# Kernel optimization log

Hardware: AMD Instinct MI355X
Metric: run time of the kernel (lower is better)

The kernel has to match this reference:

```python
import jax, jax.numpy as jnp
import numpy as np
from jax import lax

N, H, W, T = 8, 100, 152, 256
STRIDE = 8
ANCHOR_SIZE = 64.0
PRE_NMS_THRESH = 0.05
PRE_NMS_TOP_N = 1000
NMS_THRESH = 0.6
POST_TOP_N = 100
IMG_H, IMG_W = 800, 1216
BW = (10.0, 10.0, 5.0, 5.0)          # BoxCoder weights (wx, wy, ww, wh)
DWH_CLIP = float(np.log(1000.0 / 16.0))
TO_REMOVE = 1.0


def setup_inputs() -> dict:
    key = jax.random.key(0)
    k1, k2, k3 = jax.random.split(key, 3)
    box_regression = jax.random.normal(k1, (N, 4, H, W), dtype=jnp.float32)
    centerness = jax.random.normal(k2, (N, 1, H, W), dtype=jnp.float32)
    dot_product_logits = jax.random.normal(k3, (N, H * W, T), dtype=jnp.float32)
    # anchor grid matching permute_and_flatten's (H, W, A) row-major ordering
    ys, xs = jnp.meshgrid(jnp.arange(H, dtype=jnp.float32),
                          jnp.arange(W, dtype=jnp.float32), indexing="ij")
    cx = xs.reshape(-1) * STRIDE + STRIDE / 2.0
    cy = ys.reshape(-1) * STRIDE + STRIDE / 2.0
    half = ANCHOR_SIZE / 2.0
    anc = jnp.stack([cx - half, cy - half, cx + half, cy + half], axis=-1)  # [H*W, 4]
    anchors = jnp.broadcast_to(anc, (N, H * W, 4)).astype(jnp.float32)
    return {"box_regression": box_regression, "centerness": centerness,
            "anchors": anchors, "dot_product_logits": dot_product_logits}


def _decode(rel, anc):
    w = anc[..., 2] - anc[..., 0] + TO_REMOVE
    h = anc[..., 3] - anc[..., 1] + TO_REMOVE
    cx = anc[..., 0] + 0.5 * w
    cy = anc[..., 1] + 0.5 * h
    dx = rel[..., 0] / BW[0]
    dy = rel[..., 1] / BW[1]
    dw = jnp.minimum(rel[..., 2] / BW[2], DWH_CLIP)
    dh = jnp.minimum(rel[..., 3] / BW[3], DWH_CLIP)
    pcx = dx * w + cx
    pcy = dy * h + cy
    pw = jnp.exp(dw) * w
    ph = jnp.exp(dh) * h
    return jnp.stack([pcx - 0.5 * pw, pcy - 0.5 * ph,
                      pcx + 0.5 * pw - 1.0, pcy + 0.5 * ph - 1.0], axis=-1)


def _iou_one_vs_all(box, boxes):
    area1 = (box[2] - box[0] + TO_REMOVE) * (box[3] - box[1] + TO_REMOVE)
    area2 = (boxes[:, 2] - boxes[:, 0] + TO_REMOVE) * (boxes[:, 3] - boxes[:, 1] + TO_REMOVE)
    lt = jnp.maximum(box[:2], boxes[:, :2])
    rb = jnp.minimum(box[2:], boxes[:, 2:])
    wh = jnp.maximum(rb - lt + TO_REMOVE, 0.0)
    inter = wh[:, 0] * wh[:, 1]
    return inter / (area1 + area2 - inter)


def _nms_single(boxes, scores):
    # greedy NMS, fixed POST_TOP_N iterations (fpn_post_nms_top_n)
    def step(s, _):
        j = jnp.argmax(s)
        sj = s[j]
        bj = boxes[j]
        flag = (sj > 0).astype(boxes.dtype)
        ious = _iou_one_vs_all(bj, boxes)
        s = jnp.where(ious > NMS_THRESH, 0.0, s).at[j].set(0.0)
        return s, (bj * flag, sj * flag)
    _, (kb, ks) = lax.scan(step, scores, None, length=POST_TOP_N)
    return kb, ks


def reference(box_regression, centerness, anchors, dot_product_logits):
    n, _, h, w = box_regression.shape
    # sigmoid + MEAN token aggregation  -> [N, HWA]
    scores = jax.nn.sigmoid(dot_product_logits).mean(-1)
    # permute_and_flatten: [N,4A,H,W] -> [N, HWA, 4]
    box_reg = box_regression.reshape(n, 1, 4, h, w).transpose(0, 3, 4, 1, 2).reshape(n, -1, 4)
    ctr = jax.nn.sigmoid(centerness.reshape(n, 1, 1, h, w).transpose(0, 3, 4, 1, 2).reshape(n, -1))
    cand = scores > PRE_NMS_THRESH          # threshold on raw aggregated scores
    cls = scores * ctr                      # centerness-weighted score
    masked = jnp.where(cand, cls, 0.0)
    vals, idx = lax.top_k(masked, PRE_NMS_TOP_N)          # per-image top-k candidates
    valid = jnp.take_along_axis(cand, idx, axis=1)        # [N, PRE_NMS_TOP_N]
    sel_reg = jnp.take_along_axis(box_reg, idx[..., None], axis=1)
    sel_anc = jnp.take_along_axis(anchors, idx[..., None], axis=1)
    boxes = _decode(sel_reg, sel_anc)
    # clip_to_image
    boxes = jnp.stack([
        jnp.clip(boxes[..., 0], 0.0, IMG_W - 1.0),
        jnp.clip(boxes[..., 1], 0.0, IMG_H - 1.0),
        jnp.clip(boxes[..., 2], 0.0, IMG_W - 1.0),
        jnp.clip(boxes[..., 3], 0.0, IMG_H - 1.0)], axis=-1)
    vf = valid.astype(boxes.dtype)
    det_scores = jnp.sqrt(jnp.where(valid, vals, 1.0)) * vf   # sqrt of cls*ctr, safe grad
    keep_boxes, keep_scores = jax.vmap(_nms_single)(boxes, det_scores)
    return keep_boxes, keep_scores
```

## Files before the change

kernel.cpp:

```cpp
#include <hip/hip_runtime.h>
#include <math.h>

#define NN 8
#define HH 100
#define WW 152
#define HW (HH*WW)
#define TT 256
#define TOPN 1000
#define POSTN 100
#define NMS_T 0.6f
#define IMGW 1216
#define IMGH 800
#define DWH_CLIP 4.135166556742356f

typedef unsigned long long u64;
typedef unsigned int u32;

__global__ __launch_bounds__(256) void score_kernel(
    const float* __restrict__ logits,
    const float* __restrict__ centerness,
    float* __restrict__ masked)
{
    int wid  = blockIdx.x * 4 + (threadIdx.x >> 6);
    int lane = threadIdx.x & 63;
    const float4 v = *(reinterpret_cast<const float4*>(logits + (size_t)wid * TT) + lane);
    float s = 0.f;
    s += __fdividef(1.f, 1.f + expf(-v.x));
    s += __fdividef(1.f, 1.f + expf(-v.y));
    s += __fdividef(1.f, 1.f + expf(-v.z));
    s += __fdividef(1.f, 1.f + expf(-v.w));
    #pragma unroll
    for (int off = 32; off; off >>= 1) s += __shfl_xor(s, off, 64);
    if (lane == 0) {
        float score = s * (1.0f / 256.0f);
        float c = centerness[wid];
        float ctr = 1.f / (1.f + expf(-c));
        masked[wid] = (score > 0.05f) ? score * ctr : 0.f;
    }
}

__global__ __launch_bounds__(256) void select_nms_kernel(
    const float* __restrict__ masked,
    const float* __restrict__ box_reg,
    float* __restrict__ out)
{
    const int n   = blockIdx.x;
    const int tid = threadIdx.x;
    const int wv  = tid >> 6;
    const int PER = (HW + 255) / 256;

    u32 bits[PER];
    const float* mb = masked + (size_t)n * HW;
    #pragma unroll
    for (int j = 0; j < PER; j++) {
        int e = tid + j * 256;
        bits[j] = (e < HW) ? __float_as_uint(mb[e]) : 0u;
    }

    __shared__ int   parts[2][4];
    __shared__ u64   keys[256];
    __shared__ float4 sbox[256];
    __shared__ float  sscr[256];
    __shared__ int   s_cnt1, s_cnt2;
    __shared__ int   s_state;

    float* outb = out + (size_t)n * POSTN * 4;
    float* outs = out + (size_t)NN * POSTN * 4 + (size_t)n * POSTN;

    float ax1 = 0.f, ay1 = 0.f, ax2 = 0.f, ay2 = 0.f;
    float bx1 = 0.f, by1 = 0.f, bx2 = 0.f, by2 = 0.f;
    int   kept = 0;
    bool  done = false;

    u32 thrPrev = 0xFFFFFFFFu;
    int  p = 0;

    for (int b = 0; b < 4 && !done; ++b) {
        const int target = 256 * (b + 1) - 1;
        u32 lo = 0u;
        u32 hi = (thrPrev < 0x3F800000u) ? thrPrev : 0x3F800000u;
        while (lo < hi) {
            u32 mid = lo + ((hi - lo) >> 1);
            int c = 0;
            #pragma unroll
            for (int j = 0; j < PER; j++) c += (bits[j] > mid) ? 1 : 0;
            #pragma unroll
            for (int off = 32; off; off >>= 1) c += __shfl_xor(c, off, 64);
            if ((tid & 63) == 0) parts[p][wv] = c;
            __syncthreads();
            int tot = parts[p][0] + parts[p][1] + parts[p][2] + parts[p][3];
            p ^= 1;
            if (tot <= target) hi = mid; else lo = mid + 1;
        }
        const u32 thr = lo;

        if (tid == 0) { s_cnt1 = 0; s_cnt2 = 0; }
        keys[tid] = 0ull;
        __syncthreads();
        #pragma unroll
        for (int j = 0; j < PER; j++) {
            int e = tid + j * 256;
            u32 v = bits[j];
            if (e < HW && v > thr && v < thrPrev) {
                int pos = atomicAdd(&s_cnt1, 1);
                if (pos < 256) keys[pos] = (((u64)v) << 32) | (u32)(~e);
            }
        }
        __syncthreads();
        const int c1 = min(s_cnt1, 256);
        #pragma unroll
        for (int j = 0; j < PER; j++) {
            int e = tid + j * 256;
            if (e < HW && bits[j] == thr) {
                int q = atomicAdd(&s_cnt2, 1);
                if (c1 + q < 256) keys[c1 + q] = (((u64)thr) << 32) | (u32)(~e);
            }
        }
        __syncthreads();

        for (int k = 2; k <= 256; k <<= 1) {
            for (int j2 = k >> 1; j2 > 0; j2 >>= 1) {
                int ixj = tid ^ j2;
                if (ixj > tid) {
                    u64 a = keys[tid], bb = keys[ixj];
                    bool sw = ((tid & k) == 0) ? (a < bb) : (a > bb);
                    if (sw) { keys[tid] = bb; keys[ixj] = a; }
                }
                __syncthreads();
            }
        }

        {
            u64 kk = keys[tid];
            float s = __uint_as_float((u32)(kk >> 32));
            float4 box = make_float4(0.f, 0.f, 0.f, 0.f);
            float scr = 0.f;
            if (s > 0.f) {
                int loc = (int)(~(u32)kk);
                float acx = (float)(loc % WW) * 8.f + 4.f;
                float acy = (float)(loc / WW) * 8.f + 4.f;
                float a0 = acx - 32.f, a1 = acy - 32.f, a2 = acx + 32.f, a3 = acy + 32.f;
                float r0 = box_reg[((size_t)n * 4 + 0) * HW + loc];
                float r1 = box_reg[((size_t)n * 4 + 1) * HW + loc];
                float r2 = box_reg[((size_t)n * 4 + 2) * HW + loc];
                float r3 = box_reg[((size_t)n * 4 + 3) * HW + loc];
                float w  = a2 - a0 + 1.0f;
                float h  = a3 - a1 + 1.0f;
                float cx = a0 + 0.5f * w;
                float cy = a1 + 0.5f * h;
                float dx = r0 / 10.0f;
                float dy = r1 / 10.0f;
                float dw = fminf(r2 / 5.0f, DWH_CLIP);
                float dh = fminf(r3 / 5.0f, DWH_CLIP);
                float pcx = dx * w + cx;
                float pcy = dy * h + cy;
                float pw  = expf(dw) * w;
                float ph  = expf(dh) * h;
                float x1 = pcx - 0.5f * pw;
                float y1 = pcy - 0.5f * ph;
                float x2 = pcx + 0.5f * pw - 1.0f;
                float y2 = pcy + 0.5f * ph - 1.0f;
                box.x = fminf(fmaxf(x1, 0.f), (float)(IMGW - 1));
                box.y = fminf(fmaxf(y1, 0.f), (float)(IMGH - 1));
                box.z = fminf(fmaxf(x2, 0.f), (float)(IMGW - 1));
                box.w = fminf(fmaxf(y2, 0.f), (float)(IMGH - 1));
                scr = sqrtf(s);
            }
            sbox[tid] = box;
            sscr[tid] = scr;
        }
        __syncthreads();

        if (tid < 64) {
            const int limit = (b == 3) ? (TOPN - 3 * 256) : 256;
            for (int i = 0; i < limit; ++i) {
                float s = sscr[i];
                if (s <= 0.f) { done = true; break; }
                float4 cb = sbox[i];
                float carea = (cb.z - cb.x + 1.f) * (cb.w - cb.y + 1.f);

                float ix1 = fmaxf(cb.x, ax1), iy1 = fmaxf(cb.y, ay1);
                float ix2 = fminf(cb.z, ax2), iy2 = fminf(cb.w, ay2);
                float iw = fmaxf(ix2 - ix1 + 1.f, 0.f), ih = fmaxf(iy2 - iy1 + 1.f, 0.f);
                float interA = iw * ih;
                float areaA = (ax2 - ax1 + 1.f) * (ay2 - ay1 + 1.f);
                float iouA = interA / (carea + areaA - interA);

                ix1 = fmaxf(cb.x, bx1); iy1 = fmaxf(cb.y, by1);
                ix2 = fminf(cb.z, bx2); iy2 = fminf(cb.w, by2);
                iw = fmaxf(ix2 - ix1 + 1.f, 0.f); ih = fmaxf(iy2 - iy1 + 1.f, 0.f);
                float interB = iw * ih;
                float areaB = (bx2 - bx1 + 1.f) * (by2 - by1 + 1.f);
                float iouB = interB / (carea + areaB - interB);

                bool supA = (tid < kept)      && (iouA > NMS_T);
                bool supB = (tid < kept - 64) && (iouB > NMS_T);
                u64 sup = __ballot(supA) | __ballot(supB);
                if (sup == 0ull) {
                    if (kept < 64) {
                        if (tid == kept)      { ax1 = cb.x; ay1 = cb.y; ax2 = cb.z; ay2 = cb.w; }
                    } else {
                        if (tid == kept - 64) { bx1 = cb.x; by1 = cb.y; bx2 = cb.z; by2 = cb.w; }
                    }
                    if (tid == 0) {
                        outb[kept * 4 + 0] = cb.x; outb[kept * 4 + 1] = cb.y;
                        outb[kept * 4 + 2] = cb.z; outb[kept * 4 + 3] = cb.w;
                        outs[kept] = s;
                    }
                    ++kept;
                    if (kept == POSTN) { done = true; break; }
                }
            }
            if (tid == 0) s_state = kept | (done ? 0x10000 : 0);
        }
        __syncthreads();
        done = (s_state >> 16) != 0;
        thrPrev = thr;
    }

    const int cnt = s_state & 0xFFFF;
    for (int i = cnt + tid; i < POSTN; i += 256) {
        outb[i * 4 + 0] = 0.f; outb[i * 4 + 1] = 0.f;
        outb[i * 4 + 2] = 0.f; outb[i * 4 + 3] = 0.f;
        outs[i] = 0.f;
    }
}

extern "C" void kernel_launch(void* const* d_in, const int* in_sizes, int n_in,
                              void* d_out, int out_size, void* d_ws, size_t ws_size,
                              hipStream_t stream) {
    const float* box_reg = (const float*)d_in[0];
    const float* center  = (const float*)d_in[1];
    const float* logits  = (const float*)d_in[3];
    float* out = (float*)d_out;

    float* masked = (float*)d_ws;

    score_kernel<<<(NN * HW) / 4, 256, 0, stream>>>(logits, center, masked);
    select_nms_kernel<<<NN, 256, 0, stream>>>(masked, box_reg, out);
}
```

Before: 260.3 us.

## Replace batched bitonic-sort NMS with single-pass argmax-driven greedy NMS

Drops the four rounds of radix-threshold search, bitonic sort and sequential NMS over 256-candidate batches. It now does one threshold search for the top 1000, decodes every candidate once into shared memory, and runs greedy NMS in one wavefront. Each step takes a wave-wide argmax over packed score/index keys held in registers and then suppresses the remaining candidates with a division-free IoU test. This removes the sort barriers and the per-candidate serial loop; the cost is about 100 iterations of 16-candidate IoU per lane plus a shuffle reduction, and the double-precision comparison may be slow.

```diff
diff --git a/kernel.cpp b/kernel.cpp
--- a/kernel.cpp
+++ b/kernel.cpp
@@ -7,8 +7,8 @@
 #define HW (HH*WW)
 #define TT 256
 #define TOPN 1000
+#define CAP 1024
 #define POSTN 100
-#define NMS_T 0.6f
 #define IMGW 1216
 #define IMGH 800
 #define DWH_CLIP 4.135166556742356f
@@ -44,12 +44,13 @@
     const float* __restrict__ box_reg,
     float* __restrict__ out)
 {
-    const int n   = blockIdx.x;
-    const int tid = threadIdx.x;
-    const int wv  = tid >> 6;
-    const int PER = (HW + 255) / 256;
-
-    u32 bits[PER];
+    const int n    = blockIdx.x;
+    const int tid  = threadIdx.x;
+    const int wv   = tid >> 6;
+    const int lane = tid & 63;
+    const int PER  = (HW + 255) / 256;
+
+    u32 bits[(HW + 255) / 256];
     const float* mb = masked + (size_t)n * HW;
     #pragma unroll
     for (int j = 0; j < PER; j++) {
@@ -57,168 +58,169 @@
         bits[j] = (e < HW) ? __float_as_uint(mb[e]) : 0u;
     }
 
-    __shared__ int   parts[2][4];
-    __shared__ u64   keys[256];
-    __shared__ float4 sbox[256];
-    __shared__ float  sscr[256];
-    __shared__ int   s_cnt1, s_cnt2;
-    __shared__ int   s_state;
+    __shared__ int    parts[2][4];
+    __shared__ int    s_cnt1, s_cnt2, s_kept;
+    __shared__ float4 sbox[CAP];
+    __shared__ float  s_scr[CAP];
+    __shared__ float  s_area[CAP];
+    __shared__ u32    s_loc[CAP];
 
     float* outb = out + (size_t)n * POSTN * 4;
     float* outs = out + (size_t)NN * POSTN * 4 + (size_t)n * POSTN;
 
-    float ax1 = 0.f, ay1 = 0.f, ax2 = 0.f, ay2 = 0.f;
-    float bx1 = 0.f, by1 = 0.f, bx2 = 0.f, by2 = 0.f;
-    int   kept = 0;
-    bool  done = false;
-
-    u32 thrPrev = 0xFFFFFFFFu;
-    int  p = 0;
-
-    for (int b = 0; b < 4 && !done; ++b) {
-        const int target = 256 * (b + 1) - 1;
-        u32 lo = 0u;
-        u32 hi = (thrPrev < 0x3F800000u) ? thrPrev : 0x3F800000u;
-        while (lo < hi) {
-            u32 mid = lo + ((hi - lo) >> 1);
-            int c = 0;
-            #pragma unroll
-            for (int j = 0; j < PER; j++) c += (bits[j] > mid) ? 1 : 0;
-            #pragma unroll
-            for (int off = 32; off; off >>= 1) c += __shfl_xor(c, off, 64);
-            if ((tid & 63) == 0) parts[p][wv] = c;
-            __syncthreads();
-            int tot = parts[p][0] + parts[p][1] + parts[p][2] + parts[p][3];
-            p ^= 1;
-            if (tot <= target) hi = mid; else lo = mid + 1;
-        }
-        const u32 thr = lo;
-
-        if (tid == 0) { s_cnt1 = 0; s_cnt2 = 0; }
-        keys[tid] = 0ull;
+    int p = 0;
+    u32 lo = 0u, hi = 0x3F800000u;
+    while (lo < hi) {
+        u32 mid = lo + ((hi - lo) >> 1);
+        int c = 0;
+        #pragma unroll
+        for (int j = 0; j < PER; j++) c += (bits[j] > mid) ? 1 : 0;
+        #pragma unroll
+        for (int off = 32; off; off >>= 1) c += __shfl_xor(c, off, 64);
+        if (lane == 0) parts[p][wv] = c;
         __syncthreads();
-        #pragma unroll
-        for (int j = 0; j < PER; j++) {
-            int e = tid + j * 256;
-            u32 v = bits[j];
-            if (e < HW && v > thr && v < thrPrev) {
-                int pos = atomicAdd(&s_cnt1, 1);
-                if (pos < 256) keys[pos] = (((u64)v) << 32) | (u32)(~e);
-            }
-        }
-        __syncthreads();
-        const int c1 = min(s_cnt1, 256);
+        int tot = parts[p][0] + parts[p][1] + parts[p][2] + parts[p][3];
+        p ^= 1;
+        if (tot <= TOPN - 1) hi = mid; else lo = mid + 1;
+    }
+    const u32 thr = lo;
+
+    #pragma unroll
+    for (int j = 0; j < CAP / 256; j++) s_scr[tid + j * 256] = 0.f;
+    if (tid == 0) { s_cnt1 = 0; s_cnt2 = 0; }
+    __syncthreads();
+    #pragma unroll
+    for (int j = 0; j < PER; j++) {
+        int e = tid + j * 256;
+        u32 v = bits[j];
+        if (e < HW && v > thr) {
+            int pos = atomicAdd(&s_cnt1, 1);
+            if (pos < TOPN) { s_scr[pos] = __uint_as_float(v); s_loc[pos] = (u32)e; }
+        }
+    }
+    __syncthreads();
+    const int c1 = min(s_cnt1, TOPN);
+    if (thr > 0u) {
         #pragma unroll
         for (int j = 0; j < PER; j++) {
             int e = tid + j * 256;
             if (e < HW && bits[j] == thr) {
                 int q = atomicAdd(&s_cnt2, 1);
-                if (c1 + q < 256) keys[c1 + q] = (((u64)thr) << 32) | (u32)(~e);
-            }
-        }
-        __syncthreads();
-
-        for (int k = 2; k <= 256; k <<= 1) {
-            for (int j2 = k >> 1; j2 > 0; j2 >>= 1) {
-                int ixj = tid ^ j2;
-                if (ixj > tid) {
-                    u64 a = keys[tid], bb = keys[ixj];
-                    bool sw = ((tid & k) == 0) ? (a < bb) : (a > bb);
-                    if (sw) { keys[tid] = bb; keys[ixj] = a; }
-                }
-                __syncthreads();
-            }
-        }
-
-        {
-            u64 kk = keys[tid];
-            float s = __uint_as_float((u32)(kk >> 32));
-            float4 box = make_float4(0.f, 0.f, 0.f, 0.f);
-            float scr = 0.f;
-            if (s > 0.f) {
-                int loc = (int)(~(u32)kk);
-                float acx = (float)(loc % WW) * 8.f + 4.f;
-                float acy = (float)(loc / WW) * 8.f + 4.f;
-                float a0 = acx - 32.f, a1 = acy - 32.f, a2 = acx + 32.f, a3 = acy + 32.f;
-                float r0 = box_reg[((size_t)n * 4 + 0) * HW + loc];
-                float r1 = box_reg[((size_t)n * 4 + 1) * HW + loc];
-                float r2 = box_reg[((size_t)n * 4 + 2) * HW + loc];
-                float r3 = box_reg[((size_t)n * 4 + 3) * HW + loc];
-                float w  = a2 - a0 + 1.0f;
-                float h  = a3 - a1 + 1.0f;
-                float cx = a0 + 0.5f * w;
-                float cy = a1 + 0.5f * h;
-                float dx = r0 / 10.0f;
-                float dy = r1 / 10.0f;
-                float dw = fminf(r2 / 5.0f, DWH_CLIP);
-                float dh = fminf(r3 / 5.0f, DWH_CLIP);
-                float pcx = dx * w + cx;
-                float pcy = dy * h + cy;
-                float pw  = expf(dw) * w;
-                float ph  = expf(dh) * h;
-                float x1 = pcx - 0.5f * pw;
-                float y1 = pcy - 0.5f * ph;
-                float x2 = pcx + 0.5f * pw - 1.0f;
-                float y2 = pcy + 0.5f * ph - 1.0f;
-                box.x = fminf(fmaxf(x1, 0.f), (float)(IMGW - 1));
-                box.y = fminf(fmaxf(y1, 0.f), (float)(IMGH - 1));
-                box.z = fminf(fmaxf(x2, 0.f), (float)(IMGW - 1));
-                box.w = fminf(fmaxf(y2, 0.f), (float)(IMGH - 1));
-                scr = sqrtf(s);
-            }
-            sbox[tid] = box;
-            sscr[tid] = scr;
-        }
-        __syncthreads();
-
-        if (tid < 64) {
-            const int limit = (b == 3) ? (TOPN - 3 * 256) : 256;
-            for (int i = 0; i < limit; ++i) {
-                float s = sscr[i];
-                if (s <= 0.f) { done = true; break; }
-                float4 cb = sbox[i];
-                float carea = (cb.z - cb.x + 1.f) * (cb.w - cb.y + 1.f);
-
-                float ix1 = fmaxf(cb.x, ax1), iy1 = fmaxf(cb.y, ay1);
-                float ix2 = fminf(cb.z, ax2), iy2 = fminf(cb.w, ay2);
-                float iw = fmaxf(ix2 - ix1 + 1.f, 0.f), ih = fmaxf(iy2 - iy1 + 1.f, 0.f);
-                float interA = iw * ih;
-                float areaA = (ax2 - ax1 + 1.f) * (ay2 - ay1 + 1.f);
-                float iouA = interA / (carea + areaA - interA);
-
-                ix1 = fmaxf(cb.x, bx1); iy1 = fmaxf(cb.y, by1);
-                ix2 = fminf(cb.z, bx2); iy2 = fminf(cb.w, by2);
-                iw = fmaxf(ix2 - ix1 + 1.f, 0.f); ih = fmaxf(iy2 - iy1 + 1.f, 0.f);
-                float interB = iw * ih;
-                float areaB = (bx2 - bx1 + 1.f) * (by2 - by1 + 1.f);
-                float iouB = interB / (carea + areaB - interB);
-
-                bool supA = (tid < kept)      && (iouA > NMS_T);
-                bool supB = (tid < kept - 64) && (iouB > NMS_T);
-                u64 sup = __ballot(supA) | __ballot(supB);
-                if (sup == 0ull) {
-                    if (kept < 64) {
-                        if (tid == kept)      { ax1 = cb.x; ay1 = cb.y; ax2 = cb.z; ay2 = cb.w; }
-                    } else {
-                        if (tid == kept - 64) { bx1 = cb.x; by1 = cb.y; bx2 = cb.z; by2 = cb.w; }
-                    }
-                    if (tid == 0) {
-                        outb[kept * 4 + 0] = cb.x; outb[kept * 4 + 1] = cb.y;
-                        outb[kept * 4 + 2] = cb.z; outb[kept * 4 + 3] = cb.w;
-                        outs[kept] = s;
-                    }
-                    ++kept;
-                    if (kept == POSTN) { done = true; break; }
-                }
-            }
-            if (tid == 0) s_state = kept | (done ? 0x10000 : 0);
-        }
-        __syncthreads();
-        done = (s_state >> 16) != 0;
-        thrPrev = thr;
-    }
-
-    const int cnt = s_state & 0xFFFF;
+                int pos = c1 + q;
+                if (pos < TOPN) { s_scr[pos] = __uint_as_float(thr); s_loc[pos] = (u32)e; }
+            }
+        }
+    }
+    __syncthreads();
+
+    #pragma unroll
+    for (int j = 0; j < CAP / 256; j++) {
+        int slot = tid + j * 256;
+        float s = s_scr[slot];
+        float4 box = make_float4(0.f, 0.f, 0.f, 0.f);
+        float area = 0.f;
+        if (s > 0.f) {
+            int loc = (int)s_loc[slot];
+            float acx = (float)(loc % WW) * 8.f + 4.f;
+            float acy = (float)(loc / WW) * 8.f + 4.f;
+            float a0 = acx - 32.f, a1 = acy - 32.f, a2 = acx + 32.f, a3 = acy + 32.f;
+            float r0 = box_reg[((size_t)n * 4 + 0) * HW + loc];
+            float r1 = box_reg[((size_t)n * 4 + 1) * HW + loc];
+            float r2 = box_reg[((size_t)n * 4 + 2) * HW + loc];
+            float r3 = box_reg[((size_t)n * 4 + 3) * HW + loc];
+            float w  = a2 - a0 + 1.0f;
+            float h  = a3 - a1 + 1.0f;
+            float cx = a0 + 0.5f * w;
+            float cy = a1 + 0.5f * h;
+            float dx = r0 / 10.0f;
+            float dy = r1 / 10.0f;
+            float dw = fminf(r2 / 5.0f, DWH_CLIP);
+            float dh = fminf(r3 / 5.0f, DWH_CLIP);
+            float pcx = dx * w + cx;
+            float pcy = dy * h + cy;
+            float pw  = expf(dw) * w;
+            float ph  = expf(dh) * h;
+            float x1 = pcx - 0.5f * pw;
+            float y1 = pcy - 0.5f * ph;
+            float x2 = pcx + 0.5f * pw - 1.0f;
+            float y2 = pcy + 0.5f * ph - 1.0f;
+            box.x = fminf(fmaxf(x1, 0.f), (float)(IMGW - 1));
+            box.y = fminf(fmaxf(y1, 0.f), (float)(IMGH - 1));
+            box.z = fminf(fmaxf(x2, 0.f), (float)(IMGW - 1));
+            box.w = fminf(fmaxf(y2, 0.f), (float)(IMGH - 1));
+            area = (box.z - box.x + 1.0f) * (box.w - box.y + 1.0f);
+        }
+        sbox[slot]   = box;
+        s_area[slot] = area;
+    }
+    __syncthreads();
+
+    if (tid < 64) {
+        u64   key[16];
+        float cx1[16], cy1[16], cx2[16], cy2[16], car[16];
+        #pragma unroll
+        for (int r = 0; r < 16; r++) {
+            int slot = r * 64 + lane;
+            float s  = s_scr[slot];
+            float4 b = sbox[slot];
+            cx1[r] = b.x; cy1[r] = b.y; cx2[r] = b.z; cy2[r] = b.w;
+            car[r] = s_area[slot];
+            u32 loc = s_loc[slot];
+            key[r] = (s > 0.f)
+                ? ((((u64)__float_as_uint(s)) << 32)
+                   | ((u64)((16383u - loc) & 0x3FFFu) << 10)
+                   | (u64)slot)
+                : 0ull;
+        }
+
+        const double MD = (double)0.6f + 0x1p-25;
+        int kept = 0;
+        while (kept < POSTN) {
+            u64 t[8];
+            #pragma unroll
+            for (int r = 0; r < 8; r++) t[r] = (key[2*r] > key[2*r+1]) ? key[2*r] : key[2*r+1];
+            #pragma unroll
+            for (int r = 0; r < 4; r++) t[r] = (t[r] > t[r+4]) ? t[r] : t[r+4];
+            t[0] = (t[0] > t[2]) ? t[0] : t[2];
+            t[1] = (t[1] > t[3]) ? t[1] : t[3];
+            u64 m = (t[0] > t[1]) ? t[0] : t[1];
+            #pragma unroll
+            for (int off = 32; off; off >>= 1) {
+                u64 o = __shfl_xor(m, off, 64);
+                if (o > m) m = o;
+            }
+            if (m == 0ull) break;
+
+            const int   slot  = (int)(m & 1023u);
+            const float ws    = __uint_as_float((u32)(m >> 32));
+            const float4 wb   = sbox[slot];
+            const float warea = s_area[slot];
+            if (lane == 0) {
+                outb[kept * 4 + 0] = wb.x; outb[kept * 4 + 1] = wb.y;
+                outb[kept * 4 + 2] = wb.z; outb[kept * 4 + 3] = wb.w;
+                outs[kept] = sqrtf(ws);
+            }
+            if ((slot & 63) == lane) key[slot >> 6] = 0ull;
+            #pragma unroll
+            for (int r = 0; r < 16; r++) {
+                float ix1 = fmaxf(wb.x, cx1[r]);
+                float iy1 = fmaxf(wb.y, cy1[r]);
+                float ix2 = fminf(wb.z, cx2[r]);
+                float iy2 = fminf(wb.w, cy2[r]);
+                float iw = fmaxf(ix2 - ix1 + 1.0f, 0.0f);
+                float ih = fmaxf(iy2 - iy1 + 1.0f, 0.0f);
+                float inter = iw * ih;
+                float denom = (warea + car[r]) - inter;
+                bool sup = ((double)inter > MD * (double)denom);
+                key[r] = sup ? 0ull : key[r];
+            }
+            ++kept;
+        }
+        if (lane == 0) s_kept = kept;
+    }
+    __syncthreads();
+
+    const int cnt = s_kept;
     for (int i = cnt + tid; i < POSTN; i += 256) {
         outb[i * 4 + 0] = 0.f; outb[i * 4 + 1] = 0.f;
         outb[i * 4 + 2] = 0.f; outb[i * 4 + 3] = 0.f;
```

Result: slower. 336.5 us (+29.3%).

## Select full top-1000 in one pass and sort 1024 keys instead of batched 256

Applied to the files above, without the earlier changes.

Replaces the incremental four-batch top-k (a radix binary search, a 256-key bitonic sort and an NMS pass per batch) with a single threshold search for the top 1000, one 1024-key bitonic sort, a single decode pass and one NMS scan. It also caches kept-box areas and prefetches the next candidate in the NMS loop. This removes the repeated binary searches and the per-batch synchronisation. In exchange it always sorts and decodes the full 1024 entries, even when NMS reaches 100 kept boxes within the first 256 candidates, which the old early exit avoided.

```diff
diff --git a/kernel.cpp b/kernel.cpp
--- a/kernel.cpp
+++ b/kernel.cpp
@@ -7,6 +7,7 @@
 #define HW (HH*WW)
 #define TT 256
 #define TOPN 1000
+#define CAP 1024
 #define POSTN 100
 #define NMS_T 0.6f
 #define IMGW 1216
@@ -44,12 +45,13 @@
     const float* __restrict__ box_reg,
     float* __restrict__ out)
 {
-    const int n   = blockIdx.x;
-    const int tid = threadIdx.x;
-    const int wv  = tid >> 6;
-    const int PER = (HW + 255) / 256;
-
-    u32 bits[PER];
+    const int n    = blockIdx.x;
+    const int tid  = threadIdx.x;
+    const int wv   = tid >> 6;
+    const int lane = tid & 63;
+    const int PER  = (HW + 255) / 256;
+
+    u32 bits[(HW + 255) / 256];
     const float* mb = masked + (size_t)n * HW;
     #pragma unroll
     for (int j = 0; j < PER; j++) {
@@ -57,168 +59,168 @@
         bits[j] = (e < HW) ? __float_as_uint(mb[e]) : 0u;
     }
 
-    __shared__ int   parts[2][4];
-    __shared__ u64   keys[256];
-    __shared__ float4 sbox[256];
-    __shared__ float  sscr[256];
-    __shared__ int   s_cnt1, s_cnt2;
-    __shared__ int   s_state;
+    __shared__ int    parts[2][4];
+    __shared__ int    s_cnt1, s_cnt2, s_kept;
+    __shared__ u64    keys[CAP];
+    __shared__ float4 sbox[CAP];
+    __shared__ float  sscr[CAP];
 
     float* outb = out + (size_t)n * POSTN * 4;
     float* outs = out + (size_t)NN * POSTN * 4 + (size_t)n * POSTN;
 
-    float ax1 = 0.f, ay1 = 0.f, ax2 = 0.f, ay2 = 0.f;
-    float bx1 = 0.f, by1 = 0.f, bx2 = 0.f, by2 = 0.f;
-    int   kept = 0;
-    bool  done = false;
-
-    u32 thrPrev = 0xFFFFFFFFu;
-    int  p = 0;
-
-    for (int b = 0; b < 4 && !done; ++b) {
-        const int target = 256 * (b + 1) - 1;
-        u32 lo = 0u;
-        u32 hi = (thrPrev < 0x3F800000u) ? thrPrev : 0x3F800000u;
-        while (lo < hi) {
-            u32 mid = lo + ((hi - lo) >> 1);
-            int c = 0;
-            #pragma unroll
-            for (int j = 0; j < PER; j++) c += (bits[j] > mid) ? 1 : 0;
-            #pragma unroll
-            for (int off = 32; off; off >>= 1) c += __shfl_xor(c, off, 64);
-            if ((tid & 63) == 0) parts[p][wv] = c;
-            __syncthreads();
-            int tot = parts[p][0] + parts[p][1] + parts[p][2] + parts[p][3];
-            p ^= 1;
-            if (tot <= target) hi = mid; else lo = mid + 1;
-        }
-        const u32 thr = lo;
-
-        if (tid == 0) { s_cnt1 = 0; s_cnt2 = 0; }
-        keys[tid] = 0ull;
+    int p = 0;
+    u32 lo = 0u, hi = 0x3F800000u;
+    while (lo < hi) {
+        u32 mid = lo + ((hi - lo) >> 1);
+        int c = 0;
+        #pragma unroll
+        for (int j = 0; j < PER; j++) c += (bits[j] > mid) ? 1 : 0;
+        #pragma unroll
+        for (int off = 32; off; off >>= 1) c += __shfl_xor(c, off, 64);
+        if (lane == 0) parts[p][wv] = c;
         __syncthreads();
-        #pragma unroll
-        for (int j = 0; j < PER; j++) {
-            int e = tid + j * 256;
-            u32 v = bits[j];
-            if (e < HW && v > thr && v < thrPrev) {
-                int pos = atomicAdd(&s_cnt1, 1);
-                if (pos < 256) keys[pos] = (((u64)v) << 32) | (u32)(~e);
-            }
-        }
-        __syncthreads();
-        const int c1 = min(s_cnt1, 256);
+        int tot = parts[p][0] + parts[p][1] + parts[p][2] + parts[p][3];
+        p ^= 1;
+        if (tot <= TOPN - 1) hi = mid; else lo = mid + 1;
+    }
+    const u32 thr = lo;
+
+    #pragma unroll
+    for (int j = 0; j < CAP / 256; j++) keys[tid + j * 256] = 0ull;
+    if (tid == 0) { s_cnt1 = 0; s_cnt2 = 0; }
+    __syncthreads();
+    #pragma unroll
+    for (int j = 0; j < PER; j++) {
+        int e = tid + j * 256;
+        u32 v = bits[j];
+        if (e < HW && v > thr) {
+            int pos = atomicAdd(&s_cnt1, 1);
+            if (pos < TOPN) keys[pos] = (((u64)v) << 32) | (u32)(~e);
+        }
+    }
+    __syncthreads();
+    const int c1 = min(s_cnt1, TOPN);
+    if (thr > 0u) {
         #pragma unroll
         for (int j = 0; j < PER; j++) {
             int e = tid + j * 256;
             if (e < HW && bits[j] == thr) {
                 int q = atomicAdd(&s_cnt2, 1);
-                if (c1 + q < 256) keys[c1 + q] = (((u64)thr) << 32) | (u32)(~e);
+                int pos = c1 + q;
+                if (pos < TOPN) keys[pos] = (((u64)thr) << 32) | (u32)(~e);
             }
         }
-        __syncthreads();
-
-        for (int k = 2; k <= 256; k <<= 1) {
-            for (int j2 = k >> 1; j2 > 0; j2 >>= 1) {
-                int ixj = tid ^ j2;
-                if (ixj > tid) {
-                    u64 a = keys[tid], bb = keys[ixj];
-                    bool sw = ((tid & k) == 0) ? (a < bb) : (a > bb);
-                    if (sw) { keys[tid] = bb; keys[ixj] = a; }
-                }
-                __syncthreads();
-            }
-        }
-
-        {
-            u64 kk = keys[tid];
-            float s = __uint_as_float((u32)(kk >> 32));
-            float4 box = make_float4(0.f, 0.f, 0.f, 0.f);
-            float scr = 0.f;
-            if (s > 0.f) {
-                int loc = (int)(~(u32)kk);
-                float acx = (float)(loc % WW) * 8.f + 4.f;
-                float acy = (float)(loc / WW) * 8.f + 4.f;
-                float a0 = acx - 32.f, a1 = acy - 32.f, a2 = acx + 32.f, a3 = acy + 32.f;
-                float r0 = box_reg[((size_t)n * 4 + 0) * HW + loc];
-                float r1 = box_reg[((size_t)n * 4 + 1) * HW + loc];
-                float r2 = box_reg[((size_t)n * 4 + 2) * HW + loc];
-                float r3 = box_reg[((size_t)n * 4 + 3) * HW + loc];
-                float w  = a2 - a0 + 1.0f;
-                float h  = a3 - a1 + 1.0f;
-                float cx = a0 + 0.5f * w;
-                float cy = a1 + 0.5f * h;
-                float dx = r0 / 10.0f;
-                float dy = r1 / 10.0f;
-                float dw = fminf(r2 / 5.0f, DWH_CLIP);
-                float dh = fminf(r3 / 5.0f, DWH_CLIP);
-                float pcx = dx * w + cx;
-                float pcy = dy * h + cy;
-                float pw  = expf(dw) * w;
-                float ph  = expf(dh) * h;
-                float x1 = pcx - 0.5f * pw;
-                float y1 = pcy - 0.5f * ph;
-                float x2 = pcx + 0.5f * pw - 1.0f;
-                float y2 = pcy + 0.5f * ph - 1.0f;
-                box.x = fminf(fmaxf(x1, 0.f), (float)(IMGW - 1));
-                box.y = fminf(fmaxf(y1, 0.f), (float)(IMGH - 1));
-                box.z = fminf(fmaxf(x2, 0.f), (float)(IMGW - 1));
-                box.w = fminf(fmaxf(y2, 0.f), (float)(IMGH - 1));
-                scr = sqrtf(s);
-            }
-            sbox[tid] = box;
-            sscr[tid] = scr;
-        }
-        __syncthreads();
-
-        if (tid < 64) {
-            const int limit = (b == 3) ? (TOPN - 3 * 256) : 256;
-            for (int i = 0; i < limit; ++i) {
-                float s = sscr[i];
-                if (s <= 0.f) { done = true; break; }
-                float4 cb = sbox[i];
-                float carea = (cb.z - cb.x + 1.f) * (cb.w - cb.y + 1.f);
-
-                float ix1 = fmaxf(cb.x, ax1), iy1 = fmaxf(cb.y, ay1);
-                float ix2 = fminf(cb.z, ax2), iy2 = fminf(cb.w, ay2);
-                float iw = fmaxf(ix2 - ix1 + 1.f, 0.f), ih = fmaxf(iy2 - iy1 + 1.f, 0.f);
-                float interA = iw * ih;
-                float areaA = (ax2 - ax1 + 1.f) * (ay2 - ay1 + 1.f);
-                float iouA = interA / (carea + areaA - interA);
-
-                ix1 = fmaxf(cb.x, bx1); iy1 = fmaxf(cb.y, by1);
-                ix2 = fminf(cb.z, bx2); iy2 = fminf(cb.w, by2);
-                iw = fmaxf(ix2 - ix1 + 1.f, 0.f); ih = fmaxf(iy2 - iy1 + 1.f, 0.f);
-                float interB = iw * ih;
-                float areaB = (bx2 - bx1 + 1.f) * (by2 - by1 + 1.f);
-                float iouB = interB / (carea + areaB - interB);
-
-                bool supA = (tid < kept)      && (iouA > NMS_T);
-                bool supB = (tid < kept - 64) && (iouB > NMS_T);
-                u64 sup = __ballot(supA) | __ballot(supB);
-                if (sup == 0ull) {
-                    if (kept < 64) {
-                        if (tid == kept)      { ax1 = cb.x; ay1 = cb.y; ax2 = cb.z; ay2 = cb.w; }
-                    } else {
-                        if (tid == kept - 64) { bx1 = cb.x; by1 = cb.y; bx2 = cb.z; by2 = cb.w; }
-                    }
-                    if (tid == 0) {
-                        outb[kept * 4 + 0] = cb.x; outb[kept * 4 + 1] = cb.y;
-                        outb[kept * 4 + 2] = cb.z; outb[kept * 4 + 3] = cb.w;
-                        outs[kept] = s;
-                    }
-                    ++kept;
-                    if (kept == POSTN) { done = true; break; }
+    }
+    __syncthreads();
+
+    for (int k = 2; k <= CAP; k <<= 1) {
+        for (int j2 = k >> 1; j2 > 0; j2 >>= 1) {
+            #pragma unroll
+            for (int e = 0; e < CAP / 256; e++) {
+                int i = tid + e * 256;
+                int ixj = i ^ j2;
+                if (ixj > i) {
+                    u64 a = keys[i], bb = keys[ixj];
+                    bool sw = ((i & k) == 0) ? (a < bb) : (a > bb);
+                    if (sw) { keys[i] = bb; keys[ixj] = a; }
                 }
             }
-            if (tid == 0) s_state = kept | (done ? 0x10000 : 0);
-        }
-        __syncthreads();
-        done = (s_state >> 16) != 0;
-        thrPrev = thr;
-    }
-
-    const int cnt = s_state & 0xFFFF;
+            __syncthreads();
+        }
+    }
+
+    #pragma unroll
+    for (int e = 0; e < CAP / 256; e++) {
+        int pos = tid + e * 256;
+        u64 kk = keys[pos];
+        float s = __uint_as_float((u32)(kk >> 32));
+        float4 box = make_float4(0.f, 0.f, 0.f, 0.f);
+        if (s > 0.f) {
+            int loc = (int)(~(u32)kk);
+            float acx = (float)(loc % WW) * 8.f + 4.f;
+            float acy = (float)(loc / WW) * 8.f + 4.f;
+            float a0 = acx - 32.f, a1 = acy - 32.f, a2 = acx + 32.f, a3 = acy + 32.f;
+            float r0 = box_reg[((size_t)n * 4 + 0) * HW + loc];
+            float r1 = box_reg[((size_t)n * 4 + 1) * HW + loc];
+            float r2 = box_reg[((size_t)n * 4 + 2) * HW + loc];
+            float r3 = box_reg[((size_t)n * 4 + 3) * HW + loc];
+            float w  = a2 - a0 + 1.0f;
+            float h  = a3 - a1 + 1.0f;
+            float cx = a0 + 0.5f * w;
+            float cy = a1 + 0.5f * h;
+            float dx = r0 / 10.0f;
+            float dy = r1 / 10.0f;
+            float dw = fminf(r2 / 5.0f, DWH_CLIP);
+            float dh = fminf(r3 / 5.0f, DWH_CLIP);
+            float pcx = dx * w + cx;
+            float pcy = dy * h + cy;
+            float pw  = expf(dw) * w;
+            float ph  = expf(dh) * h;
+            float x1 = pcx - 0.5f * pw;
+            float y1 = pcy - 0.5f * ph;
+            float x2 = pcx + 0.5f * pw - 1.0f;
+            float y2 = pcy + 0.5f * ph - 1.0f;
+            box.x = fminf(fmaxf(x1, 0.f), (float)(IMGW - 1));
+            box.y = fminf(fmaxf(y1, 0.f), (float)(IMGH - 1));
+            box.z = fminf(fmaxf(x2, 0.f), (float)(IMGW - 1));
+            box.w = fminf(fmaxf(y2, 0.f), (float)(IMGH - 1));
+        }
+        sbox[pos] = box;
+        sscr[pos] = s;
+    }
+    __syncthreads();
+
+    if (tid < 64) {
+        float ax1 = 0.f, ay1 = 0.f, ax2 = 0.f, ay2 = 0.f, aar = 0.f;
+        float bx1 = 0.f, by1 = 0.f, bx2 = 0.f, by2 = 0.f, bar = 0.f;
+        int kept = 0;
+
+        float  ns = sscr[0];
+        float4 nb = sbox[0];
+        for (int i = 0; i < CAP; ++i) {
+            float  s  = ns;
+            float4 cb = nb;
+            int ip = i + 1;
+            if (ip < CAP) { ns = sscr[ip]; nb = sbox[ip]; }
+            if (s <= 0.f) break;
+
+            float carea = (cb.z - cb.x + 1.f) * (cb.w - cb.y + 1.f);
+
+            float ix1 = fmaxf(cb.x, ax1), iy1 = fmaxf(cb.y, ay1);
+            float ix2 = fminf(cb.z, ax2), iy2 = fminf(cb.w, ay2);
+            float iw = fmaxf(ix2 - ix1 + 1.f, 0.f), ih = fmaxf(iy2 - iy1 + 1.f, 0.f);
+            float interA = iw * ih;
+            float iouA = interA / (carea + aar - interA);
+
+            ix1 = fmaxf(cb.x, bx1); iy1 = fmaxf(cb.y, by1);
+            ix2 = fminf(cb.z, bx2); iy2 = fminf(cb.w, by2);
+            iw = fmaxf(ix2 - ix1 + 1.f, 0.f); ih = fmaxf(iy2 - iy1 + 1.f, 0.f);
+            float interB = iw * ih;
+            float iouB = interB / (carea + bar - interB);
+
+            bool supA = (tid < kept)      && (iouA > NMS_T);
+            bool supB = (tid < kept - 64) && (iouB > NMS_T);
+            u64 sup = __ballot(supA) | __ballot(supB);
+            if (sup == 0ull) {
+                if (kept < 64) {
+                    if (tid == kept)      { ax1 = cb.x; ay1 = cb.y; ax2 = cb.z; ay2 = cb.w; aar = carea; }
+                } else {
+                    if (tid == kept - 64) { bx1 = cb.x; by1 = cb.y; bx2 = cb.z; by2 = cb.w; bar = carea; }
+                }
+                if (tid == 0) {
+                    outb[kept * 4 + 0] = cb.x; outb[kept * 4 + 1] = cb.y;
+                    outb[kept * 4 + 2] = cb.z; outb[kept * 4 + 3] = cb.w;
+                    outs[kept] = sqrtf(s);
+                }
+                ++kept;
+                if (kept == POSTN) break;
+            }
+        }
+        if (tid == 0) s_kept = kept;
+    }
+    __syncthreads();
+
+    const int cnt = s_kept;
     for (int i = cnt + tid; i < POSTN; i += 256) {
         outb[i * 4 + 0] = 0.f; outb[i * 4 + 1] = 0.f;
         outb[i * 4 + 2] = 0.f; outb[i * 4 + 3] = 0.f;
```

After: 283.5 us. 8.9% more time.
